# Kernel optimization log

Hardware: AMD Instinct MI355X
Metric: run time of the kernel (lower is better)

The kernel has to match this reference:

```python
import jax, jax.numpy as jnp
import numpy as np

B, C = 4096, 10000


def setup_inputs() -> dict:
    key = jax.random.key(0)
    k1, k2, k3, k4, k5 = jax.random.split(key, 5)
    return {
        "outputs1": jax.random.normal(k1, (B, C), jnp.float32),
        "outputs2": jax.random.normal(k2, (B, C), jnp.float32),
        "outputs3": jax.random.normal(k3, (B, C), jnp.float32),
        "out_s": jax.random.normal(k4, (B, C), jnp.float32),
        "targets": jax.random.randint(k5, (B,), 0, C),
    }


def _margin(out, targets):
    # top1 - top2 if the target class is the argmax, else 0  -> [B]
    top2 = jax.lax.top_k(out, 2)[0]                              # [B, 2]
    tgt = jnp.take_along_axis(out, targets[:, None], axis=1)[:, 0]
    return jnp.where(tgt == top2[:, 0], top2[:, 0] - top2[:, 1], jnp.zeros_like(tgt))


def reference(outputs1, outputs2, outputs3, out_s, targets):
    T_THR = 2.0   # Threshold_weights3 temperature
    T_KD = 20.0   # KL_divergence temperature
    ALPHA = 0.8

    mimic = (outputs1 + outputs2 + outputs3) / 3.0
    teachers = (outputs1, outputs2, outputs3, mimic)

    # per-sample confidence margins for each teacher -> softmax ensemble weights [B,4]
    d = jnp.stack([_margin(t, targets) for t in teachers], axis=1)
    out_threshold = jax.nn.softmax(d / T_THR, axis=1)

    # global max over the three real teachers (scalar)
    max_preds = jnp.maximum(jnp.max(outputs1), jnp.maximum(jnp.max(outputs2), jnp.max(outputs3)))

    # per-sample student CE (shared across teachers)
    ce = -jnp.take_along_axis(jax.nn.log_softmax(out_s, axis=1), targets[:, None], axis=1)[:, 0]
    logp_s = jax.nn.log_softmax(out_s / T_KD, axis=1)

    def loss_for(teacher):
        w = jnp.take_along_axis(teacher, targets[:, None], axis=1)[:, 0] / max_preds
        kd = -jnp.sum(jax.nn.softmax(teacher / T_KD, axis=1) * logp_s, axis=1) * (T_KD * T_KD)
        return (1.0 - ALPHA * w) * ce + (ALPHA * w) * kd

    losses = jnp.stack([loss_for(t) for t in teachers], axis=1)  # [B,4]
    return jnp.mean(jnp.sum(out_threshold * losses, axis=1))
```

## Files before the change

### kernel.cpp

```cpp
#include <hip/hip_runtime.h>

namespace {
constexpr int kB = 4096;
constexpr int kC = 10000;
constexpr int kC4 = kC / 4;
constexpr int kNT = 256;
}

__device__ __forceinline__ float wave_sum(float v) {
#pragma unroll
  for (int o = 32; o > 0; o >>= 1) v += __shfl_down(v, o, 64);
  return v;
}

__device__ __forceinline__ double wave_sum_d(double v) {
#pragma unroll
  for (int o = 32; o > 0; o >>= 1) v += __shfl_down(v, o, 64);
  return v;
}

__device__ __forceinline__ float wave_max(float v) {
#pragma unroll
  for (int o = 32; o > 0; o >>= 1) v = fmaxf(v, __shfl_down(v, o, 64));
  return v;
}

__device__ __forceinline__ void wave_top2(float& m1, float& m2) {
#pragma unroll
  for (int o = 32; o > 0; o >>= 1) {
    float a1 = __shfl_down(m1, o, 64);
    float a2 = __shfl_down(m2, o, 64);
    float lo = fminf(m1, a1);
    m1 = fmaxf(m1, a1);
    m2 = fmaxf(lo, fmaxf(m2, a2));
  }
}

struct Chunk {
  float4 a, b, c, s;
};

__global__ __launch_bounds__(kNT) void mt3_row_kernel(
    const float* __restrict__ g1, const float* __restrict__ g2,
    const float* __restrict__ g3, const float* __restrict__ gs,
    const int* __restrict__ gt,
    float* __restrict__ ceArr, float* __restrict__ bArr,
    float* __restrict__ mArr) {
  const int b = blockIdx.x;
  const int tid = threadIdx.x;
  const int lane = tid & 63;
  const int wv = tid >> 6;

  const size_t rowOff = (size_t)b * kC;
  const float4* __restrict__ p1 = reinterpret_cast<const float4*>(g1 + rowOff);
  const float4* __restrict__ p2 = reinterpret_cast<const float4*>(g2 + rowOff);
  const float4* __restrict__ p3 = reinterpret_cast<const float4*>(g3 + rowOff);
  const float4* __restrict__ ps = reinterpret_cast<const float4*>(gs + rowOff);

  const int target = gt[b];

  float tv1 = 0.f, tv2 = 0.f, tv3 = 0.f, tvs = 0.f;
  if (tid == 0) {
    tv1 = g1[rowOff + target];
    tv2 = g2[rowOff + target];
    tv3 = g3[rowOff + target];
    tvs = gs[rowOff + target];
  }

  float m1[4], m2[4], Z[4], D[4];
#pragma unroll
  for (int t = 0; t < 4; t++) { m1[t] = -1e30f; m2[t] = -1e30f; Z[t] = 0.f; D[t] = 0.f; }
  float Z1 = 0.f;
  float Z20 = 0.f;

  __shared__ float sZ[4][4], sD[4][4], sM1[4][4], sM2[4][4], sZ1[4], sZ20[4];

  int c = tid;
  Chunk A0, A1, A2;
  A0.a = p1[c];        A0.b = p2[c];        A0.c = p3[c];        A0.s = ps[c];
  A1.a = p1[c + kNT];  A1.b = p2[c + kNT];  A1.c = p3[c + kNT];  A1.s = ps[c + kNT];

  while (true) {
    const int cn2 = c + 2 * kNT;
    const int idx2 = (cn2 < kC4) ? cn2 : c;
    A2.a = p1[idx2];
    A2.b = p2[idx2];
    A2.c = p3[idx2];
    A2.s = ps[idx2];

    const float va[4] = {A0.a.x, A0.a.y, A0.a.z, A0.a.w};
    const float vb[4] = {A0.b.x, A0.b.y, A0.b.z, A0.b.w};
    const float vc[4] = {A0.c.x, A0.c.y, A0.c.z, A0.c.w};
    const float vs[4] = {A0.s.x, A0.s.y, A0.s.z, A0.s.w};
#pragma unroll
    for (int j = 0; j < 4; j++) {
      const float mim = (va[j] + vb[j] + vc[j]) * (1.0f / 3.0f);
      const float tv[4] = {va[j], vb[j], vc[j], mim};
      const float sv = vs[j];
#pragma unroll
      for (int t = 0; t < 4; t++) {
        const float x = tv[t];
        const float lo = fminf(x, m1[t]);
        m1[t] = fmaxf(x, m1[t]);
        m2[t] = fmaxf(m2[t], lo);
        const float e = __expf(x * 0.05f);
        Z[t] += e;
        D[t] = fmaf(e, sv, D[t]);
      }
      Z1 += __expf(sv);
      Z20 += __expf(sv * 0.05f);
    }

    if (c + kNT >= kC4) break;
    c += kNT;
    A0 = A1;
    A1 = A2;
  }

#pragma unroll
  for (int t = 0; t < 4; t++) {
    Z[t] = wave_sum(Z[t]);
    D[t] = wave_sum(D[t]);
    wave_top2(m1[t], m2[t]);
  }
  Z1 = wave_sum(Z1);
  Z20 = wave_sum(Z20);

  if (lane == 0) {
#pragma unroll
    for (int t = 0; t < 4; t++) {
      sZ[t][wv] = Z[t]; sD[t][wv] = D[t];
      sM1[t][wv] = m1[t]; sM2[t][wv] = m2[t];
    }
    sZ1[wv] = Z1; sZ20[wv] = Z20;
  }
  __syncthreads();

  if (tid == 0) {
    float fZ[4], fD[4], fM1[4], fM2[4];
    float fZ1 = 0.f, fZ20 = 0.f;
#pragma unroll
    for (int t = 0; t < 4; t++) { fZ[t] = 0.f; fD[t] = 0.f; fM1[t] = -1e30f; fM2[t] = -1e30f; }
#pragma unroll
    for (int w = 0; w < 4; w++) {
      fZ1 += sZ1[w]; fZ20 += sZ20[w];
#pragma unroll
      for (int t = 0; t < 4; t++) {
        fZ[t] += sZ[t][w];
        fD[t] += sD[t][w];
        const float a1 = sM1[t][w], a2 = sM2[t][w];
        const float lo = fminf(fM1[t], a1);
        fM1[t] = fmaxf(fM1[t], a1);
        fM2[t] = fmaxf(lo, fmaxf(fM2[t], a2));
      }
    }

    const float tvm = (tv1 + tv2 + tv3) * (1.0f / 3.0f);
    const float tval[4] = {tv1, tv2, tv3, tvm};

    const float ce = logf(fZ1) - tvs;
    const float lz20 = logf(fZ20);

    float d[4], kd[4];
#pragma unroll
    for (int t = 0; t < 4; t++) {
      kd[t] = 400.0f * (lz20 - fD[t] / (20.0f * fZ[t]));
      d[t] = (tval[t] == fM1[t]) ? (fM1[t] - fM2[t]) : 0.0f;
    }
    float ew[4], se = 0.f;
#pragma unroll
    for (int t = 0; t < 4; t++) { ew[t] = __expf(d[t] * 0.5f); se += ew[t]; }
    float rowB = 0.f;
#pragma unroll
    for (int t = 0; t < 4; t++) rowB += (ew[t] / se) * tval[t] * (kd[t] - ce);

    ceArr[b] = ce;
    bArr[b] = rowB;
    mArr[b] = fmaxf(fM1[0], fmaxf(fM1[1], fM1[2]));
  }
}

__global__ __launch_bounds__(256) void mt3_finalize(
    const float* __restrict__ ceArr, const float* __restrict__ bArr,
    const float* __restrict__ mArr, float* __restrict__ out) {
  const int tid = threadIdx.x;
  const int lane = tid & 63;
  const int wv = tid >> 6;

  double sc = 0.0, sb = 0.0;
  float mx = -1e30f;
  for (int i = tid; i < kB; i += 256) {
    sc += (double)ceArr[i];
    sb += (double)bArr[i];
    mx = fmaxf(mx, mArr[i]);
  }
  sc = wave_sum_d(sc);
  sb = wave_sum_d(sb);
  mx = wave_max(mx);

  __shared__ double dsc[4], dsb[4];
  __shared__ float dmx[4];
  if (lane == 0) { dsc[wv] = sc; dsb[wv] = sb; dmx[wv] = mx; }
  __syncthreads();
  if (tid == 0) {
    double A = 0.0, Bc = 0.0;
    float M = -1e30f;
#pragma unroll
    for (int w = 0; w < 4; w++) { A += dsc[w]; Bc += dsb[w]; M = fmaxf(M, dmx[w]); }
    out[0] = (float)((A + 0.8 * Bc / (double)M) / (double)kB);
  }
}

extern "C" void kernel_launch(void* const* d_in, const int* in_sizes, int n_in,
                              void* d_out, int out_size, void* d_ws, size_t ws_size,
                              hipStream_t stream) {
  const float* o1 = (const float*)d_in[0];
  const float* o2 = (const float*)d_in[1];
  const float* o3 = (const float*)d_in[2];
  const float* os = (const float*)d_in[3];
  const int* tg = (const int*)d_in[4];

  float* ws = (float*)d_ws;
  float* ceArr = ws;
  float* bArr = ws + kB;
  float* mArr = ws + 2 * kB;

  mt3_row_kernel<<<kB, kNT, 0, stream>>>(o1, o2, o3, os, tg, ceArr, bArr, mArr);
  mt3_finalize<<<1, 256, 0, stream>>>(ceArr, bArr, mArr, (float*)d_out);
}
```

Before: 523.3 us.

## Use 1024-thread blocks with fully unrolled three-chunk load per row

Each row block grows from 256 to 1024 threads, so each thread covers at most three float4 chunks per input. All loads are issued up front and the rolling software pipeline loop is removed. This puts more memory requests in flight per row and drops loop overhead. The costs are larger blocks with more registers per thread in total and a longer final reduction over 16 waves done by a single thread.

```diff
diff --git a/kernel.cpp b/kernel.cpp
--- a/kernel.cpp
+++ b/kernel.cpp
@@ -4,7 +4,8 @@
 constexpr int kB = 4096;
 constexpr int kC = 10000;
 constexpr int kC4 = kC / 4;
-constexpr int kNT = 256;
+constexpr int kNT = 1024;
+constexpr int kNW = kNT / 64;
 }
 
 __device__ __forceinline__ float wave_sum(float v) {
@@ -39,6 +40,33 @@
 struct Chunk {
   float4 a, b, c, s;
 };
+
+__device__ __forceinline__ void accum_chunk(
+    const Chunk& K, float (&m1)[4], float (&m2)[4], float (&Z)[4], float (&D)[4],
+    float& Z1, float& Z20) {
+  const float va[4] = {K.a.x, K.a.y, K.a.z, K.a.w};
+  const float vb[4] = {K.b.x, K.b.y, K.b.z, K.b.w};
+  const float vc[4] = {K.c.x, K.c.y, K.c.z, K.c.w};
+  const float vs[4] = {K.s.x, K.s.y, K.s.z, K.s.w};
+#pragma unroll
+  for (int j = 0; j < 4; j++) {
+    const float mim = (va[j] + vb[j] + vc[j]) * (1.0f / 3.0f);
+    const float tv[4] = {va[j], vb[j], vc[j], mim};
+    const float sv = vs[j];
+#pragma unroll
+    for (int t = 0; t < 4; t++) {
+      const float x = tv[t];
+      const float lo = fminf(x, m1[t]);
+      m1[t] = fmaxf(x, m1[t]);
+      m2[t] = fmaxf(m2[t], lo);
+      const float e = __expf(x * 0.05f);
+      Z[t] += e;
+      D[t] = fmaf(e, sv, D[t]);
+    }
+    Z1 += __expf(sv);
+    Z20 += __expf(sv * 0.05f);
+  }
+}
 
 __global__ __launch_bounds__(kNT) void mt3_row_kernel(
     const float* __restrict__ g1, const float* __restrict__ g2,
@@ -73,49 +101,20 @@
   float Z1 = 0.f;
   float Z20 = 0.f;
 
-  __shared__ float sZ[4][4], sD[4][4], sM1[4][4], sM2[4][4], sZ1[4], sZ20[4];
-
-  int c = tid;
-  Chunk A0, A1, A2;
-  A0.a = p1[c];        A0.b = p2[c];        A0.c = p3[c];        A0.s = ps[c];
-  A1.a = p1[c + kNT];  A1.b = p2[c + kNT];  A1.c = p3[c + kNT];  A1.s = ps[c + kNT];
-
-  while (true) {
-    const int cn2 = c + 2 * kNT;
-    const int idx2 = (cn2 < kC4) ? cn2 : c;
-    A2.a = p1[idx2];
-    A2.b = p2[idx2];
-    A2.c = p3[idx2];
-    A2.s = ps[idx2];
-
-    const float va[4] = {A0.a.x, A0.a.y, A0.a.z, A0.a.w};
-    const float vb[4] = {A0.b.x, A0.b.y, A0.b.z, A0.b.w};
-    const float vc[4] = {A0.c.x, A0.c.y, A0.c.z, A0.c.w};
-    const float vs[4] = {A0.s.x, A0.s.y, A0.s.z, A0.s.w};
-#pragma unroll
-    for (int j = 0; j < 4; j++) {
-      const float mim = (va[j] + vb[j] + vc[j]) * (1.0f / 3.0f);
-      const float tv[4] = {va[j], vb[j], vc[j], mim};
-      const float sv = vs[j];
-#pragma unroll
-      for (int t = 0; t < 4; t++) {
-        const float x = tv[t];
-        const float lo = fminf(x, m1[t]);
-        m1[t] = fmaxf(x, m1[t]);
-        m2[t] = fmaxf(m2[t], lo);
-        const float e = __expf(x * 0.05f);
-        Z[t] += e;
-        D[t] = fmaf(e, sv, D[t]);
-      }
-      Z1 += __expf(sv);
-      Z20 += __expf(sv * 0.05f);
-    }
-
-    if (c + kNT >= kC4) break;
-    c += kNT;
-    A0 = A1;
-    A1 = A2;
-  }
+  const int c0 = tid;
+  const int c1 = tid + kNT;
+  const int c2 = tid + 2 * kNT;
+  const bool v2 = (c2 < kC4);
+  const int c2c = v2 ? c2 : c0;
+
+  Chunk X0, X1, X2;
+  X0.a = p1[c0];  X0.b = p2[c0];  X0.c = p3[c0];  X0.s = ps[c0];
+  X1.a = p1[c1];  X1.b = p2[c1];  X1.c = p3[c1];  X1.s = ps[c1];
+  X2.a = p1[c2c]; X2.b = p2[c2c]; X2.c = p3[c2c]; X2.s = ps[c2c];
+
+  accum_chunk(X0, m1, m2, Z, D, Z1, Z20);
+  accum_chunk(X1, m1, m2, Z, D, Z1, Z20);
+  if (v2) accum_chunk(X2, m1, m2, Z, D, Z1, Z20);
 
 #pragma unroll
   for (int t = 0; t < 4; t++) {
@@ -126,6 +125,7 @@
   Z1 = wave_sum(Z1);
   Z20 = wave_sum(Z20);
 
+  __shared__ float sZ[4][kNW], sD[4][kNW], sM1[4][kNW], sM2[4][kNW], sZ1[kNW], sZ20[kNW];
   if (lane == 0) {
 #pragma unroll
     for (int t = 0; t < 4; t++) {
@@ -142,7 +142,7 @@
 #pragma unroll
     for (int t = 0; t < 4; t++) { fZ[t] = 0.f; fD[t] = 0.f; fM1[t] = -1e30f; fM2[t] = -1e30f; }
 #pragma unroll
-    for (int w = 0; w < 4; w++) {
+    for (int w = 0; w < kNW; w++) {
       fZ1 += sZ1[w]; fZ20 += sZ20[w];
 #pragma unroll
       for (int t = 0; t < 4; t++) {
```

Result: slower. 564.4 us (+7.9%).
